# Kernel optimization log

Measured on AMD Instinct MI355X. Metric: run time of the kernel, lower is better.

The kernel has to match this reference:

```python
import jax, jax.numpy as jnp
import numpy as np

IN_DIM, HIDDEN, OUT_DIM = 784, 2048, 10
BATCH = 16384
KEEP = 0.1  # 1 - sparsity


def setup_inputs() -> dict:
    key = jax.random.key(0)
    ks = jax.random.split(key, 16)
    s1 = 1.0 / np.sqrt(IN_DIM)
    sh = 1.0 / np.sqrt(HIDDEN)
    inp = {
        "x": jax.random.normal(ks[0], (BATCH, IN_DIM), dtype=jnp.float32),
        # weights stored as (out, in) like nn.Linear
        "W1": jax.random.uniform(ks[1], (HIDDEN, IN_DIM), jnp.float32, -s1, s1),
        "b1": jax.random.uniform(ks[2], (HIDDEN,), jnp.float32, -s1, s1),
        "W2": jax.random.uniform(ks[3], (HIDDEN, HIDDEN), jnp.float32, -sh, sh),
        "b2": jax.random.uniform(ks[4], (HIDDEN,), jnp.float32, -sh, sh),
        "W3": jax.random.uniform(ks[5], (HIDDEN, HIDDEN), jnp.float32, -sh, sh),
        "b3": jax.random.uniform(ks[6], (HIDDEN,), jnp.float32, -sh, sh),
        "W4": jax.random.uniform(ks[7], (HIDDEN, HIDDEN), jnp.float32, -sh, sh),
        "b4": jax.random.uniform(ks[8], (HIDDEN,), jnp.float32, -sh, sh),
        "W5": jax.random.uniform(ks[9], (OUT_DIM, HIDDEN), jnp.float32, -sh, sh),
        "b5": jax.random.uniform(ks[10], (OUT_DIM,), jnp.float32, -sh, sh),
        "m1": jax.random.bernoulli(ks[11], KEEP, (HIDDEN, IN_DIM)),
        "m2": jax.random.bernoulli(ks[12], KEEP, (HIDDEN, HIDDEN)),
        "m3": jax.random.bernoulli(ks[13], KEEP, (HIDDEN, HIDDEN)),
        "m4": jax.random.bernoulli(ks[14], KEEP, (HIDDEN, HIDDEN)),
    }
    return inp


def _sparse_linear(x, W, b, m):
    # masked linear: y = x @ (W*m)^T + b
    Wm = W * m.astype(W.dtype)
    return x @ Wm.T + b


def reference(x, W1, b1, W2, b2, W3, b3, W4, b4, W5, b5, m1, m2, m3, m4):
    h = x.reshape(x.shape[0], -1)
    h = jax.nn.relu(_sparse_linear(h, W1, b1, m1))
    h = jax.nn.relu(_sparse_linear(h, W2, b2, m2))
    h = jax.nn.relu(_sparse_linear(h, W3, b3, m3))
    h = jax.nn.relu(_sparse_linear(h, W4, b4, m4))
    return h @ W5.T + b5
```

## Files before the change

kernel.cpp:

```cpp
#include <hip/hip_runtime.h>
#include <hip/hip_bf16.h>
#include <hip/hip_fp16.h>

#define BATCH 16384
#define HID   2048
#define IND   784
#define INDP  896
#define OUTD  10

typedef _Float16 f16;
typedef __attribute__((ext_vector_type(8))) _Float16 f16x8;
typedef __attribute__((ext_vector_type(4))) _Float16 f16x4;
typedef __attribute__((ext_vector_type(4))) float f32x4;

struct PrepArgs {
    const float* src[6];
    const void*  mk[6];
    f16*         dst[6];
    long         off4[7];
    int          rin[6], kin[6], kout[6];
};

__global__ void prep_fused(PrepArgs a, long total4) {
    long idx = (long)blockIdx.x * blockDim.x + threadIdx.x;
    if (idx >= total4) return;
    int s = 0;
    #pragma unroll
    for (int i = 1; i < 6; ++i) s += (idx >= a.off4[i]);
    long li = idx - a.off4[s];
    int kout = a.kout[s], kin = a.kin[s], rin = a.rin[s];
    int k4 = kout >> 2;
    int r = (int)(li / k4), c = (int)(li - (long)r * k4) << 2;
    f16x4 o = {};
    if (r < rin && c < kin) {
        float4 v = *(const float4*)(a.src[s] + (size_t)r * kin + c);
        float vv0 = v.x, vv1 = v.y, vv2 = v.z, vv3 = v.w;
        if (a.mk[s]) {
            uint4 m = *(const uint4*)((const unsigned int*)a.mk[s] + (size_t)r * kin + c);
            if (!m.x) vv0 = 0.f; if (!m.y) vv1 = 0.f;
            if (!m.z) vv2 = 0.f; if (!m.w) vv3 = 0.f;
        }
        o[0] = (f16)vv0; o[1] = (f16)vv1; o[2] = (f16)vv2; o[3] = (f16)vv3;
    }
    *(f16x4*)(a.dst[s] + (size_t)r * kout + c) = o;
}

__device__ __forceinline__ void gload_lds16(const f16* g, f16* l) {
    __builtin_amdgcn_global_load_lds(
        (const __attribute__((address_space(1))) unsigned int*)g,
        (__attribute__((address_space(3))) unsigned int*)l,
        16, 0, 0);
}

#define BAR()    __builtin_amdgcn_s_barrier()
#define SCHED()  __builtin_amdgcn_sched_barrier(0)
#define WAITV4() asm volatile("s_waitcnt vmcnt(4)" ::: "memory")
#define WAITV8() asm volatile("s_waitcnt vmcnt(8)" ::: "memory")

template<bool RELU>
__global__ __launch_bounds__(512, 2) void gemm8p(
    const f16* __restrict__ A, const f16* __restrict__ B,
    const float* __restrict__ bias, f16* __restrict__ C,
    int N, int K) {
    __shared__ f16 As[2 * 2 * 256 * 32];
    __shared__ f16 Bs[2 * 2 * 256 * 32];

    int nbn = N >> 8;
    int nwg = gridDim.x;
    int cpx = nwg >> 3;
    int bid = blockIdx.x;
    int swz = (bid & 7) * cpx + (bid >> 3);
    int bm = swz / nbn, bn = swz % nbn;

    int tid = threadIdx.x;
    int w = tid >> 6, lane = tid & 63;
    int wr = w >> 2, wc = w & 3;
    int l15 = lane & 15, l4 = lane >> 4;

    const f16* Ag = A + (size_t)bm * 256 * K;
    const f16* Bg = B + (size_t)bn * 256 * K;

    int r0 = tid >> 2, s0 = tid & 3;
    int c0 = (s0 ^ ((r0 >> 1) & 3)) * 8;
    int ldsw0 = (w * 64) * 8;
    int ldsw1 = (512 + w * 64) * 8;

    auto stageA = [&](int buf, int ks, int tk) {
        gload_lds16(Ag + (size_t)r0 * K + tk * 64 + ks * 32 + c0,
                    As + (buf * 2 + ks) * 8192 + ldsw0);
        gload_lds16(Ag + (size_t)(128 + r0) * K + tk * 64 + ks * 32 + c0,
                    As + (buf * 2 + ks) * 8192 + ldsw1);
    };
    auto stageB = [&](int buf, int ks, int tk) {
        gload_lds16(Bg + (size_t)r0 * K + tk * 64 + ks * 32 + c0,
                    Bs + (buf * 2 + ks) * 8192 + ldsw0);
        gload_lds16(Bg + (size_t)(128 + r0) * K + tk * 64 + ks * 32 + c0,
                    Bs + (buf * 2 + ks) * 8192 + ldsw1);
    };

    int rsw = (l4 ^ ((l15 >> 1) & 3)) * 8;
    auto ldA = [&](f16x8 (&af)[4], int buf, int ks, int mh) {
        int base = (buf * 2 + ks) * 8192;
        #pragma unroll
        for (int m = 0; m < 4; ++m) {
            int row = wr * 128 + (mh * 4 + m) * 16 + l15;
            af[m] = *(const f16x8*)(As + base + row * 32 + rsw);
        }
    };
    auto ldB = [&](f16x8 (&bf)[4], int buf, int ks) {
        int base = (buf * 2 + ks) * 8192;
        #pragma unroll
        for (int n = 0; n < 4; ++n) {
            int row = wc * 64 + n * 16 + l15;
            bf[n] = *(const f16x8*)(Bs + base + row * 32 + rsw);
        }
    };

    f32x4 acc[8][4] = {};
    auto mma = [&](f16x8 (&af)[4], f16x8 (&bf)[4], int mh) {
        #pragma unroll
        for (int m = 0; m < 4; ++m)
            #pragma unroll
            for (int n = 0; n < 4; ++n)
                acc[mh * 4 + m][n] = __builtin_amdgcn_mfma_f32_16x16x32_f16(
                    af[m], bf[n], acc[mh * 4 + m][n], 0, 0, 0);
    };

    int NT = K >> 6, NI = NT >> 1;

    f16x8 Aa[4], Ab[4], Ba[4], Bb[4];

    stageA(0, 0, 0); stageB(0, 0, 0); stageA(0, 1, 0); stageB(0, 1, 0);
    stageA(1, 0, 1); stageB(1, 0, 1);
    WAITV8(); SCHED(); BAR();
    ldA(Aa, 0, 0, 0); ldB(Bb, 0, 0); ldA(Ab, 0, 0, 1);
    WAITV4(); SCHED(); BAR();

    for (int it = 0; it < NI; ++it) {
        int t1 = 2 * it + 1, t2 = 2 * it + 2, t3 = 2 * it + 3;
        if (t2 >= NT) t2 = 0;
        if (t3 >= NT) t3 = 0;

        mma(Aa, Bb, 0);
        ldA(Aa, 0, 1, 0); ldB(Ba, 0, 1); stageA(1, 1, t1);
        SCHED(); BAR();
        mma(Ab, Bb, 1);
        ldA(Ab, 0, 1, 1); stageB(1, 1, t1);
        WAITV4(); SCHED(); BAR();
        mma(Aa, Ba, 0);
        ldA(Aa, 1, 0, 0); ldB(Bb, 1, 0); stageA(0, 0, t2);
        SCHED(); BAR();
        mma(Ab, Ba, 1);
        ldA(Ab, 1, 0, 1); stageB(0, 0, t2);
        WAITV4(); SCHED(); BAR();
        mma(Aa, Bb, 0);
        ldA(Aa, 1, 1, 0); ldB(Ba, 1, 1); stageA(0, 1, t2);
        SCHED(); BAR();
        mma(Ab, Bb, 1);
        ldA(Ab, 1, 1, 1); stageB(0, 1, t2);
        WAITV4(); SCHED(); BAR();
        mma(Aa, Ba, 0);
        ldA(Aa, 0, 0, 0); ldB(Bb, 0, 0); stageA(1, 0, t3);
        SCHED(); BAR();
        mma(Ab, Ba, 1);
        ldA(Ab, 0, 0, 1); stageB(1, 0, t3);
        WAITV4(); SCHED(); BAR();
    }

    #pragma unroll
    for (int nf = 0; nf < 4; ++nf) {
        int j = bn * 256 + wc * 64 + nf * 16 + l15;
        float bv = bias[j];
        #pragma unroll
        for (int mf = 0; mf < 8; ++mf) {
            int i0 = bm * 256 + wr * 128 + mf * 16 + l4 * 4;
            #pragma unroll
            for (int r = 0; r < 4; ++r) {
                float v = acc[mf][nf][r] + bv;
                if (RELU) v = fmaxf(v, 0.f);
                C[(size_t)(i0 + r) * N + j] = (f16)v;
            }
        }
    }
}

__global__ __launch_bounds__(256, 3) void gemm_head(
    const f16* __restrict__ A, const f16* __restrict__ B,
    const float* __restrict__ bias, float* __restrict__ C,
    int K, int Nout) {
    __shared__ f16 As[128 * 64];
    __shared__ f16 Bs[128 * 64];
    int bm = blockIdx.x;
    int t = threadIdx.x;
    int w = t >> 6, lane = t & 63;
    int wm = w >> 1, wn = w & 1;
    int l15 = lane & 15, l4 = lane >> 4;
    const f16* Ag = A + (size_t)bm * 128 * K;
    const f16* Bg = B;
    int rr = w * 8 + (lane >> 3);
    int cc = (lane & 7) * 8;
    f32x4 acc[4][4] = {};
    for (int k0 = 0; k0 < K; k0 += 64) {
        #pragma unroll
        for (int i = 0; i < 4; ++i)
            gload_lds16(Ag + (size_t)(i * 32 + rr) * K + k0 + cc, As + i * 2048 + w * 512);
        #pragma unroll
        for (int i = 0; i < 4; ++i)
            gload_lds16(Bg + (size_t)(i * 32 + rr) * K + k0 + cc, Bs + i * 2048 + w * 512);
        __syncthreads();
        #pragma unroll
        for (int ks = 0; ks < 2; ++ks) {
            f16x8 af[4], bfr[4];
            #pragma unroll
            for (int m = 0; m < 4; ++m)
                af[m] = *(const f16x8*)(As + (wm * 64 + m * 16 + l15) * 64 + ks * 32 + l4 * 8);
            #pragma unroll
            for (int n = 0; n < 4; ++n)
                bfr[n] = *(const f16x8*)(Bs + (wn * 64 + n * 16 + l15) * 64 + ks * 32 + l4 * 8);
            #pragma unroll
            for (int m = 0; m < 4; ++m)
                #pragma unroll
                for (int n = 0; n < 4; ++n)
                    acc[m][n] = __builtin_amdgcn_mfma_f32_16x16x32_f16(af[m], bfr[n], acc[m][n], 0, 0, 0);
        }
        __syncthreads();
    }
    #pragma unroll
    for (int n = 0; n < 4; ++n) {
        int j = wn * 64 + n * 16 + l15;
        bool jok = j < Nout;
        float bv = jok ? bias[j] : 0.f;
        #pragma unroll
        for (int m = 0; m < 4; ++m) {
            int i0 = bm * 128 + wm * 64 + m * 16 + l4 * 4;
            #pragma unroll
            for (int r = 0; r < 4; ++r) {
                if (jok) C[(size_t)(i0 + r) * Nout + j] = acc[m][n][r] + bv;
            }
        }
    }
}

extern "C" void kernel_launch(void* const* d_in, const int* in_sizes, int n_in,
                              void* d_out, int out_size, void* d_ws, size_t ws_size,
                              hipStream_t stream) {
    const float* x  = (const float*)d_in[0];
    const float* W1 = (const float*)d_in[1];
    const float* b1 = (const float*)d_in[2];
    const float* W2 = (const float*)d_in[3];
    const float* b2 = (const float*)d_in[4];
    const float* W3 = (const float*)d_in[5];
    const float* b3 = (const float*)d_in[6];
    const float* W4 = (const float*)d_in[7];
    const float* b4 = (const float*)d_in[8];
    const float* W5 = (const float*)d_in[9];
    const float* b5 = (const float*)d_in[10];
    const void* m1 = d_in[11];
    const void* m2 = d_in[12];
    const void* m3 = d_in[13];
    const void* m4 = d_in[14];

    char* ws = (char*)d_ws;
    size_t off = 0;
    auto alloc = [&](size_t b) { char* p = ws + off; off += (b + 255) & ~(size_t)255; return p; };
    f16* xb  = (f16*)alloc((size_t)BATCH * INDP * 2);
    f16* w1b = (f16*)alloc((size_t)HID * INDP * 2);
    f16* w2b = (f16*)alloc((size_t)HID * HID * 2);
    f16* w3b = (f16*)alloc((size_t)HID * HID * 2);
    f16* w4b = (f16*)alloc((size_t)HID * HID * 2);
    f16* w5b = (f16*)alloc((size_t)128 * HID * 2);
    f16* h1  = (f16*)alloc((size_t)BATCH * HID * 2);
    f16* h2  = (f16*)alloc((size_t)BATCH * HID * 2);

    PrepArgs pa;
    auto seg = [&](int i, const float* s, const void* mk, f16* d,
                   int rin, int kin, int kout) {
        pa.src[i] = s; pa.mk[i] = mk; pa.dst[i] = d;
        pa.rin[i] = rin; pa.kin[i] = kin; pa.kout[i] = kout;
    };
    seg(0, x,  nullptr, xb,  BATCH, IND, INDP);
    seg(1, W1, m1,      w1b, HID,   IND, INDP);
    seg(2, W2, m2,      w2b, HID,   HID, HID);
    seg(3, W3, m3,      w3b, HID,   HID, HID);
    seg(4, W4, m4,      w4b, HID,   HID, HID);
    seg(5, W5, nullptr, w5b, OUTD,  HID, HID);
    long rout[6] = {BATCH, HID, HID, HID, HID, 128};
    long acc4 = 0;
    for (int i = 0; i < 6; ++i) { pa.off4[i] = acc4; acc4 += rout[i] * (pa.kout[i] >> 2); }
    pa.off4[6] = acc4;
    int pgrid = (int)((acc4 + 255) / 256);
    prep_fused<<<pgrid, 256, 0, stream>>>(pa, acc4);

    int g8 = (BATCH / 256) * (HID / 256);
    gemm8p<true><<<g8, 512, 0, stream>>>(xb, w1b, b1, h1, HID, INDP);
    gemm8p<true><<<g8, 512, 0, stream>>>(h1, w2b, b2, h2, HID, HID);
    gemm8p<true><<<g8, 512, 0, stream>>>(h2, w3b, b3, h1, HID, HID);
    gemm8p<true><<<g8, 512, 0, stream>>>(h1, w4b, b4, h2, HID, HID);
    gemm_head<<<BATCH / 128, 256, 0, stream>>>(h2, w5b, b5, (float*)d_out, HID, OUTD);
}
```

Measured before the change: 488.4 us.

## Restructure GEMM LDS layout to 64-wide K tiles with 8-phase ping-pong schedule

Changes the LDS staging from two 32-wide K halves per buffer to row-halves with full 64-wide K rows, using an XOR swizzle over 8 slots. The main loop becomes an 8-phase schedule that interleaves LDS fragment loads, async global-to-LDS staging and MFMA blocks, each separated by barriers and lgkmcnt waits. MFMA blocks run at raised wave priority via s_setprio. The intent is better overlap of memory and compute and fewer bank conflicts. In exchange it adds many more barriers per iteration, and the staggered A/B buffer timing needs careful correctness.

```diff
diff --git a/kernel.cpp b/kernel.cpp
--- a/kernel.cpp
+++ b/kernel.cpp
@@ -55,15 +55,16 @@
 #define BAR()    __builtin_amdgcn_s_barrier()
 #define SCHED()  __builtin_amdgcn_sched_barrier(0)
 #define WAITV4() asm volatile("s_waitcnt vmcnt(4)" ::: "memory")
-#define WAITV8() asm volatile("s_waitcnt vmcnt(8)" ::: "memory")
+#define WAITV2() asm volatile("s_waitcnt vmcnt(2)" ::: "memory")
+#define WAITL0() asm volatile("s_waitcnt lgkmcnt(0)" ::: "memory")
 
 template<bool RELU>
 __global__ __launch_bounds__(512, 2) void gemm8p(
     const f16* __restrict__ A, const f16* __restrict__ B,
     const float* __restrict__ bias, f16* __restrict__ C,
     int N, int K) {
-    __shared__ f16 As[2 * 2 * 256 * 32];
-    __shared__ f16 Bs[2 * 2 * 256 * 32];
+    __shared__ f16 As[2 * 2 * 128 * 64];
+    __shared__ f16 Bs[2 * 2 * 128 * 64];
 
     int nbn = N >> 8;
     int nwg = gridDim.x;
@@ -80,60 +81,63 @@
     const f16* Ag = A + (size_t)bm * 256 * K;
     const f16* Bg = B + (size_t)bn * 256 * K;
 
-    int r0 = tid >> 2, s0 = tid & 3;
-    int c0 = (s0 ^ ((r0 >> 1) & 3)) * 8;
-    int ldsw0 = (w * 64) * 8;
-    int ldsw1 = (512 + w * 64) * 8;
-
-    auto stageA = [&](int buf, int ks, int tk) {
-        gload_lds16(Ag + (size_t)r0 * K + tk * 64 + ks * 32 + c0,
-                    As + (buf * 2 + ks) * 8192 + ldsw0);
-        gload_lds16(Ag + (size_t)(128 + r0) * K + tk * 64 + ks * 32 + c0,
-                    As + (buf * 2 + ks) * 8192 + ldsw1);
-    };
-    auto stageB = [&](int buf, int ks, int tk) {
-        gload_lds16(Bg + (size_t)r0 * K + tk * 64 + ks * 32 + c0,
-                    Bs + (buf * 2 + ks) * 8192 + ldsw0);
-        gload_lds16(Bg + (size_t)(128 + r0) * K + tk * 64 + ks * 32 + c0,
-                    Bs + (buf * 2 + ks) * 8192 + ldsw1);
-    };
-
-    int rsw = (l4 ^ ((l15 >> 1) & 3)) * 8;
-    auto ldA = [&](f16x8 (&af)[4], int buf, int ks, int mh) {
-        int base = (buf * 2 + ks) * 8192;
-        #pragma unroll
-        for (int m = 0; m < 4; ++m) {
-            int row = wr * 128 + (mh * 4 + m) * 16 + l15;
-            af[m] = *(const f16x8*)(As + base + row * 32 + rsw);
-        }
-    };
-    auto ldB = [&](f16x8 (&bf)[4], int buf, int ks) {
-        int base = (buf * 2 + ks) * 8192;
-        #pragma unroll
-        for (int n = 0; n < 4; ++n) {
-            int row = wc * 64 + n * 16 + l15;
-            bf[n] = *(const f16x8*)(Bs + base + row * 32 + rsw);
-        }
+    int rr = w * 8 + (lane >> 3);
+    int gcol = ((lane & 7) ^ (lane >> 3)) * 8;
+
+    auto stageA = [&](int buf, int half, int tk) {
+        f16* l = As + (buf * 2 + half) * 8192 + (w * 64) * 8;
+        gload_lds16(Ag + (size_t)(half * 128 + rr) * K + tk * 64 + gcol, l);
+        gload_lds16(Ag + (size_t)(half * 128 + 64 + rr) * K + tk * 64 + gcol, l + 4096);
+    };
+    auto stageB = [&](int buf, int half, int tk) {
+        f16* l = Bs + (buf * 2 + half) * 8192 + (w * 64) * 8;
+        gload_lds16(Bg + (size_t)(half * 128 + rr) * K + tk * 64 + gcol, l);
+        gload_lds16(Bg + (size_t)(half * 128 + 64 + rr) * K + tk * 64 + gcol, l + 4096);
+    };
+
+    auto ldA = [&](f16x8 (&ar)[8], int buf, int mh) {
+        int base = (buf * 2 + wr) * 8192;
+        #pragma unroll
+        for (int m = 0; m < 4; ++m)
+            #pragma unroll
+            for (int ks = 0; ks < 2; ++ks) {
+                int lr = mh * 64 + m * 16 + l15;
+                int slot = (ks * 4 + l4) ^ (lr & 7);
+                ar[m * 2 + ks] = *(const f16x8*)(As + base + lr * 64 + slot * 8);
+            }
+    };
+    auto ldB = [&](f16x8 (&br)[4], int buf, int nh) {
+        int base = (buf * 2 + (wc >> 1)) * 8192;
+        #pragma unroll
+        for (int n = 0; n < 2; ++n)
+            #pragma unroll
+            for (int ks = 0; ks < 2; ++ks) {
+                int lr = (wc & 1) * 64 + nh * 32 + n * 16 + l15;
+                int slot = (ks * 4 + l4) ^ (lr & 7);
+                br[n * 2 + ks] = *(const f16x8*)(Bs + base + lr * 64 + slot * 8);
+            }
     };
 
     f32x4 acc[8][4] = {};
-    auto mma = [&](f16x8 (&af)[4], f16x8 (&bf)[4], int mh) {
+    auto mma = [&](f16x8 (&ar)[8], f16x8 (&br)[4], int mh, int nh) {
+        __builtin_amdgcn_s_setprio(1);
         #pragma unroll
         for (int m = 0; m < 4; ++m)
             #pragma unroll
-            for (int n = 0; n < 4; ++n)
-                acc[mh * 4 + m][n] = __builtin_amdgcn_mfma_f32_16x16x32_f16(
-                    af[m], bf[n], acc[mh * 4 + m][n], 0, 0, 0);
+            for (int n = 0; n < 2; ++n)
+                #pragma unroll
+                for (int ks = 0; ks < 2; ++ks)
+                    acc[mh * 4 + m][nh * 2 + n] = __builtin_amdgcn_mfma_f32_16x16x32_f16(
+                        ar[m * 2 + ks], br[n * 2 + ks], acc[mh * 4 + m][nh * 2 + n], 0, 0, 0);
+        __builtin_amdgcn_s_setprio(0);
     };
 
     int NT = K >> 6, NI = NT >> 1;
 
-    f16x8 Aa[4], Ab[4], Ba[4], Bb[4];
-
-    stageA(0, 0, 0); stageB(0, 0, 0); stageA(0, 1, 0); stageB(0, 1, 0);
-    stageA(1, 0, 1); stageB(1, 0, 1);
-    WAITV8(); SCHED(); BAR();
-    ldA(Aa, 0, 0, 0); ldB(Bb, 0, 0); ldA(Ab, 0, 0, 1);
+    f16x8 Ar[8], B0[4], B1[4];
+
+    stageA(0, 0, 0); stageA(0, 1, 0); stageB(0, 0, 0); stageB(0, 1, 0);
+    stageB(1, 0, 1); stageB(1, 1, 1);
     WAITV4(); SCHED(); BAR();
 
     for (int it = 0; it < NI; ++it) {
@@ -141,30 +145,30 @@
         if (t2 >= NT) t2 = 0;
         if (t3 >= NT) t3 = 0;
 
-        mma(Aa, Bb, 0);
-        ldA(Aa, 0, 1, 0); ldB(Ba, 0, 1); stageA(1, 1, t1);
-        SCHED(); BAR();
-        mma(Ab, Bb, 1);
-        ldA(Ab, 0, 1, 1); stageB(1, 1, t1);
-        WAITV4(); SCHED(); BAR();
-        mma(Aa, Ba, 0);
-        ldA(Aa, 1, 0, 0); ldB(Bb, 1, 0); stageA(0, 0, t2);
-        SCHED(); BAR();
-        mma(Ab, Ba, 1);
-        ldA(Ab, 1, 0, 1); stageB(0, 0, t2);
-        WAITV4(); SCHED(); BAR();
-        mma(Aa, Bb, 0);
-        ldA(Aa, 1, 1, 0); ldB(Ba, 1, 1); stageA(0, 1, t2);
-        SCHED(); BAR();
-        mma(Ab, Bb, 1);
-        ldA(Ab, 1, 1, 1); stageB(0, 1, t2);
-        WAITV4(); SCHED(); BAR();
-        mma(Aa, Ba, 0);
-        ldA(Aa, 0, 0, 0); ldB(Bb, 0, 0); stageA(1, 0, t3);
-        SCHED(); BAR();
-        mma(Ab, Ba, 1);
-        ldA(Ab, 0, 0, 1); stageB(1, 0, t3);
-        WAITV4(); SCHED(); BAR();
+        ldA(Ar, 0, 0); ldB(B0, 0, 0); stageA(1, 0, t1);
+        BAR(); WAITL0(); SCHED();
+        mma(Ar, B0, 0, 0); BAR();
+        ldB(B1, 0, 1); stageA(1, 1, t1);
+        BAR(); WAITL0(); SCHED();
+        mma(Ar, B1, 0, 1); BAR();
+        ldA(Ar, 0, 1); stageB(0, 0, t2);
+        BAR(); WAITL0(); SCHED();
+        mma(Ar, B1, 1, 1); BAR();
+        stageB(0, 1, t2);
+        BAR(); WAITL0(); SCHED();
+        mma(Ar, B0, 1, 0); WAITV4(); SCHED(); BAR();
+        ldA(Ar, 1, 0); ldB(B0, 1, 0); stageA(0, 0, t2);
+        BAR(); WAITL0(); SCHED();
+        mma(Ar, B0, 0, 0); BAR();
+        ldB(B1, 1, 1); stageA(0, 1, t2);
+        BAR(); WAITL0(); SCHED();
+        mma(Ar, B1, 0, 1); BAR();
+        ldA(Ar, 1, 1); stageB(1, 0, t3);
+        BAR(); WAITL0(); SCHED();
+        mma(Ar, B1, 1, 1); BAR();
+        stageB(1, 1, t3);
+        BAR(); WAITL0(); SCHED();
+        mma(Ar, B0, 1, 0); WAITV2(); SCHED(); BAR();
     }
 
     #pragma unroll
```

After: 512.7 us. 5.0% more time.

## Restructure GEMM main loop to process full 64-wide K tiles per MMA phase

Applied to the files above, without the earlier changes.

Reorganizes the software pipeline so each LDS fragment load and MFMA phase covers both 32-wide K halves of a 64-wide tile, halving the number of barrier phases per iteration. Staging now issues whole-tile A/B loads per phase, with a vmcnt(0) wait. This cuts barriers and phase overhead but doubles fragment register usage (8 f16x8 per operand array), which risks spills under the 512x2 launch bound. It also shortens the overlap between global loads and compute.

```diff
diff --git a/kernel.cpp b/kernel.cpp
--- a/kernel.cpp
+++ b/kernel.cpp
@@ -54,6 +54,7 @@
 
 #define BAR()    __builtin_amdgcn_s_barrier()
 #define SCHED()  __builtin_amdgcn_sched_barrier(0)
+#define WAITV0() asm volatile("s_waitcnt vmcnt(0)" ::: "memory")
 #define WAITV4() asm volatile("s_waitcnt vmcnt(4)" ::: "memory")
 #define WAITV8() asm volatile("s_waitcnt vmcnt(8)" ::: "memory")
 
@@ -99,72 +100,64 @@
     };
 
     int rsw = (l4 ^ ((l15 >> 1) & 3)) * 8;
-    auto ldA = [&](f16x8 (&af)[4], int buf, int ks, int mh) {
-        int base = (buf * 2 + ks) * 8192;
-        #pragma unroll
-        for (int m = 0; m < 4; ++m) {
-            int row = wr * 128 + (mh * 4 + m) * 16 + l15;
-            af[m] = *(const f16x8*)(As + base + row * 32 + rsw);
-        }
-    };
-    auto ldB = [&](f16x8 (&bf)[4], int buf, int ks) {
-        int base = (buf * 2 + ks) * 8192;
-        #pragma unroll
-        for (int n = 0; n < 4; ++n) {
-            int row = wc * 64 + n * 16 + l15;
-            bf[n] = *(const f16x8*)(Bs + base + row * 32 + rsw);
-        }
+    auto ldA8 = [&](f16x8 (&af)[8], int buf, int mh) {
+        #pragma unroll
+        for (int m = 0; m < 4; ++m)
+            #pragma unroll
+            for (int ks = 0; ks < 2; ++ks) {
+                int row = wr * 128 + (mh * 4 + m) * 16 + l15;
+                af[m * 2 + ks] = *(const f16x8*)(As + (buf * 2 + ks) * 8192 + row * 32 + rsw);
+            }
+    };
+    auto ldB8 = [&](f16x8 (&bf)[8], int buf) {
+        #pragma unroll
+        for (int n = 0; n < 4; ++n)
+            #pragma unroll
+            for (int ks = 0; ks < 2; ++ks) {
+                int row = wc * 64 + n * 16 + l15;
+                bf[n * 2 + ks] = *(const f16x8*)(Bs + (buf * 2 + ks) * 8192 + row * 32 + rsw);
+            }
     };
 
     f32x4 acc[8][4] = {};
-    auto mma = [&](f16x8 (&af)[4], f16x8 (&bf)[4], int mh) {
+    auto mma8 = [&](f16x8 (&af)[8], f16x8 (&bf)[8], int mh) {
         #pragma unroll
         for (int m = 0; m < 4; ++m)
             #pragma unroll
             for (int n = 0; n < 4; ++n)
-                acc[mh * 4 + m][n] = __builtin_amdgcn_mfma_f32_16x16x32_f16(
-                    af[m], bf[n], acc[mh * 4 + m][n], 0, 0, 0);
+                #pragma unroll
+                for (int ks = 0; ks < 2; ++ks)
+                    acc[mh * 4 + m][n] = __builtin_amdgcn_mfma_f32_16x16x32_f16(
+                        af[m * 2 + ks], bf[n * 2 + ks], acc[mh * 4 + m][n], 0, 0, 0);
     };
 
     int NT = K >> 6, NI = NT >> 1;
 
-    f16x8 Aa[4], Ab[4], Ba[4], Bb[4];
-
-    stageA(0, 0, 0); stageB(0, 0, 0); stageA(0, 1, 0); stageB(0, 1, 0);
-    stageA(1, 0, 1); stageB(1, 0, 1);
+    f16x8 Aa[8], Ab[8], Ba[8], Bb[8];
+
+    stageA(0, 0, 0); stageA(0, 1, 0); stageB(0, 0, 0); stageB(0, 1, 0);
+    stageA(1, 0, 1); stageA(1, 1, 1); stageB(1, 0, 1); stageB(1, 1, 1);
     WAITV8(); SCHED(); BAR();
-    ldA(Aa, 0, 0, 0); ldB(Bb, 0, 0); ldA(Ab, 0, 0, 1);
-    WAITV4(); SCHED(); BAR();
+    ldB8(Ba, 0);
 
     for (int it = 0; it < NI; ++it) {
-        int t1 = 2 * it + 1, t2 = 2 * it + 2, t3 = 2 * it + 3;
+        int t2 = 2 * it + 2, t3 = 2 * it + 3;
         if (t2 >= NT) t2 = 0;
         if (t3 >= NT) t3 = 0;
 
-        mma(Aa, Bb, 0);
-        ldA(Aa, 0, 1, 0); ldB(Ba, 0, 1); stageA(1, 1, t1);
+        ldA8(Aa, 0, 0); ldA8(Ab, 0, 1);
+        mma8(Aa, Ba, 0);
+        WAITV0(); SCHED(); BAR();
+        mma8(Ab, Ba, 1);
+        ldA8(Aa, 1, 0); ldB8(Bb, 1); stageB(0, 0, t2); stageB(0, 1, t2);
         SCHED(); BAR();
-        mma(Ab, Bb, 1);
-        ldA(Ab, 0, 1, 1); stageB(1, 1, t1);
+        mma8(Aa, Bb, 0);
+        ldA8(Ab, 1, 1); stageA(0, 0, t2); stageA(0, 1, t2);
         WAITV4(); SCHED(); BAR();
-        mma(Aa, Ba, 0);
-        ldA(Aa, 1, 0, 0); ldB(Bb, 1, 0); stageA(0, 0, t2);
-        SCHED(); BAR();
-        mma(Ab, Ba, 1);
-        ldA(Ab, 1, 0, 1); stageB(0, 0, t2);
-        WAITV4(); SCHED(); BAR();
-        mma(Aa, Bb, 0);
-        ldA(Aa, 1, 1, 0); ldB(Ba, 1, 1); stageA(0, 1, t2);
-        SCHED(); BAR();
-        mma(Ab, Bb, 1);
-        ldA(Ab, 1, 1, 1); stageB(0, 1, t2);
-        WAITV4(); SCHED(); BAR();
-        mma(Aa, Ba, 0);
-        ldA(Aa, 0, 0, 0); ldB(Bb, 0, 0); stageA(1, 0, t3);
-        SCHED(); BAR();
-        mma(Ab, Ba, 1);
-        ldA(Ab, 0, 0, 1); stageB(1, 0, t3);
-        WAITV4(); SCHED(); BAR();
+        mma8(Ab, Bb, 1);
+        ldB8(Ba, 0);
+        stageA(1, 0, t3); stageA(1, 1, t3); stageB(1, 0, t3); stageB(1, 1, t3);
+        WAITV8(); SCHED(); BAR();
     }
 
     #pragma unroll
```

After: 507.6 us. +3.9%, slower.
